# Kernel optimization log

Hardware: AMD Instinct MI355X
Metric: run time of the kernel (lower is better)

## Reference

```python
import jax, jax.numpy as jnp
import numpy as np

N = 8          # num merged RadialMLPs (experts)
D_IN = 64      # in_features
H = 128        # hidden_features
D_OUT = 64     # out_features
E = 100000     # num edges
LN_EPS = 1e-5


def setup_inputs() -> dict:
    key = jax.random.key(0)
    ks = jax.random.split(key, 12)
    s = lambda *shape: 0.05
    return {
        "x": jax.random.normal(ks[0], (E, D_IN), dtype=jnp.float32),
        # first layer concatenated across experts: [N*H, D_IN]
        "W1_cat": jax.random.normal(ks[1], (N * H, D_IN), dtype=jnp.float32) * 0.05,
        "b1_cat": jax.random.normal(ks[2], (N * H,), dtype=jnp.float32) * 0.05,
        "gamma1": jnp.ones((N, H), dtype=jnp.float32),
        "beta1": jnp.zeros((N, H), dtype=jnp.float32),
        "W2": jax.random.normal(ks[3], (N, H, H), dtype=jnp.float32) * 0.05,
        "b2": jax.random.normal(ks[4], (N, H), dtype=jnp.float32) * 0.05,
        "gamma2": jnp.ones((N, H), dtype=jnp.float32),
        "beta2": jnp.zeros((N, H), dtype=jnp.float32),
        "W3": jax.random.normal(ks[5], (N, D_OUT, H), dtype=jnp.float32) * 0.05,
        "b3": jax.random.normal(ks[6], (N, D_OUT), dtype=jnp.float32) * 0.05,
    }


def _layer_norm(h, gamma, beta):
    # h: [E, N, H]; gamma/beta: [N, H]; normalize over last dim (biased var)
    mu = jnp.mean(h, axis=-1, keepdims=True)
    var = jnp.mean(jnp.square(h - mu), axis=-1, keepdims=True)
    hn = (h - mu) * jax.lax.rsqrt(var + LN_EPS)
    return hn * gamma[None, :, :] + beta[None, :, :]


def reference(x, W1_cat, b1_cat, gamma1, beta1, W2, b2, gamma2, beta2, W3, b3):
    # Shared first GEMM: [E, D_IN] x [D_IN, N*H] -> [E, N, H]
    h = (x @ W1_cat.T + b1_cat).reshape(x.shape[0], N, H)
    h = jax.nn.silu(_layer_norm(h, gamma1, beta1))
    # Per-expert Linear 2, batched: W2 is [N, H_out, H_in]
    h = jnp.einsum("enh,nkh->enk", h, W2) + b2[None, :, :]
    h = jax.nn.silu(_layer_norm(h, gamma2, beta2))
    # Per-expert Linear 3: W3 is [N, D_OUT, H]
    out = jnp.einsum("enh,noh->eno", h, W3) + b3[None, :, :]
    # [N, E, D_OUT]: stack of the N per-expert outputs (original returns a list)
    return jnp.transpose(out, (1, 0, 2))
```

## Files before the change

kernel.cpp:

```cpp
#include <hip/hip_runtime.h>

#define NEXP 8
#define E_TOT 100000
#define EPB 64
#define NTILE 1563

typedef __bf16 bf16x8 __attribute__((ext_vector_type(8)));
typedef float f32x4 __attribute__((ext_vector_type(4)));
typedef unsigned short u16x8 __attribute__((ext_vector_type(8)));

union BF8 { u16x8 u; bf16x8 b; };
union BW  { __bf16 h; unsigned short u; };

__device__ __forceinline__ unsigned short f2bf(float f) {
  unsigned int u = __float_as_uint(f);
  u += 0x7fffu + ((u >> 16) & 1u);
  return (unsigned short)(u >> 16);
}

__device__ __forceinline__ int sidx(int r, int c, int stride) {
  return r * stride + (c ^ ((r & 7) << 3));
}

__device__ __forceinline__ bf16x8 fragld(const unsigned short* a, int off) {
  BF8 t;
  t.u = *(const u16x8*)(a + off);
  return t.b;
}

__device__ __forceinline__ bf16x8 frag_f32(const float* s) {
  float4 u0 = *(const float4*)s;
  float4 u1 = *(const float4*)(s + 4);
  BF8 t;
  t.u[0]=f2bf(u0.x); t.u[1]=f2bf(u0.y); t.u[2]=f2bf(u0.z); t.u[3]=f2bf(u0.w);
  t.u[4]=f2bf(u1.x); t.u[5]=f2bf(u1.y); t.u[6]=f2bf(u1.z); t.u[7]=f2bf(u1.w);
  return t.b;
}

__global__ void k_conv_w(const float* __restrict__ W1c, const float* __restrict__ W2p,
                         const float* __restrict__ W3p, unsigned short* __restrict__ wsW) {
  int gid = blockIdx.x * 256 + threadIdx.x;
  int n = gid >> 15, p = gid & 32767;
  int idx, frag, t, s;
  const float* base;
  int K;
  if (p < 8192)       { idx = p;         frag = idx >> 9; t = frag >> 1; s = frag & 1;
                        base = W1c + (size_t)n * 8192;  K = 64; }
  else if (p < 24576) { idx = p - 8192;  frag = idx >> 9; t = frag >> 2; s = frag & 3;
                        base = W2p + (size_t)n * 16384; K = 128; }
  else                { idx = p - 24576; frag = idx >> 9; t = frag >> 2; s = frag & 3;
                        base = W3p + (size_t)n * 8192;  K = 128; }
  int r = idx & 511, lane = r >> 3, j = r & 7;
  int l15 = lane & 15, gq = lane >> 4;
  wsW[gid] = f2bf(base[(16 * t + l15) * K + 32 * s + 8 * gq + j]);
}

__global__ void k_conv_x(const float* __restrict__ xg, unsigned short* __restrict__ xb) {
  int gid = blockIdx.x * 256 + threadIdx.x;
  const float* s = xg + (size_t)gid * 8;
  BF8 t;
  float4 a = *(const float4*)s, b = *(const float4*)(s + 4);
  t.u[0]=f2bf(a.x); t.u[1]=f2bf(a.y); t.u[2]=f2bf(a.z); t.u[3]=f2bf(a.w);
  t.u[4]=f2bf(b.x); t.u[5]=f2bf(b.y); t.u[6]=f2bf(b.z); t.u[7]=f2bf(b.w);
  *(u16x8*)(xb + (size_t)gid * 8) = t.u;
}

template <bool USEWS>
__global__ __launch_bounds__(256, 3) void k_main(
    const unsigned short* __restrict__ wsW, const unsigned short* __restrict__ xb,
    const float* __restrict__ xg,
    const float* __restrict__ W1c, const float* __restrict__ b1c,
    const float* __restrict__ g1p, const float* __restrict__ bt1p,
    const float* __restrict__ W2p, const float* __restrict__ b2p,
    const float* __restrict__ g2p, const float* __restrict__ bt2p,
    const float* __restrict__ W3p, const float* __restrict__ b3p,
    float* __restrict__ outp)
{
  __shared__ __attribute__((aligned(16))) unsigned short hs[EPB * 128];
  __shared__ __attribute__((aligned(16))) float prm[832];

  const int bid = blockIdx.x;
  const int g_  = (bid & 7) * NTILE + (bid >> 3);
  const int tile = g_ >> 3;
  const int n    = g_ & 7;
  const int e0   = tile * EPB;

  const int tid  = threadIdx.x;
  const int lane = tid & 63;
  const int wv   = tid >> 6;
  const int l15  = lane & 15;
  const int gq   = lane >> 4;
  const int wrow = wv * 16;

  for (int i = tid; i < 832; i += 256) {
    int grp = i >> 7, f = i & 127;
    float v;
    switch (grp) {
      case 0: v = b1c [n * 128 + f]; break;
      case 1: v = g1p [n * 128 + f]; break;
      case 2: v = bt1p[n * 128 + f]; break;
      case 3: v = b2p [n * 128 + f]; break;
      case 4: v = g2p [n * 128 + f]; break;
      case 5: v = bt2p[n * 128 + f]; break;
      default: v = b3p[n * 64 + f]; break;
    }
    prm[i] = v;
  }

  bf16x8 ax[2];
  {
    int e = e0 + wrow + l15;
    if (e >= E_TOT) e = E_TOT - 1;
    if (USEWS) {
#pragma unroll
      for (int s = 0; s < 2; ++s)
        ax[s] = fragld(xb, e * 64 + s * 32 + 8 * gq);
    } else {
#pragma unroll
      for (int s = 0; s < 2; ++s)
        ax[s] = frag_f32(xg + (size_t)e * 64 + s * 32 + 8 * gq);
    }
  }

  const unsigned short* wf1 = wsW + (size_t)n * 32768;
  const unsigned short* wf2 = wf1 + 8192;
  const unsigned short* wf3 = wf1 + 24576;
  const float* W1n = W1c + (size_t)n * 8192;
  const float* W2n = W2p + (size_t)n * 16384;
  const float* W3n = W3p + (size_t)n * 8192;

  auto wfragA = [&](const unsigned short* wf, const float* Wn, int nfs, int t, int s, int K) {
    if (USEWS) return fragld(wf, ((t * nfs + s) << 9) + (lane << 3));
    return frag_f32(Wn + (16 * t + l15) * K + 32 * s + 8 * gq);
  };

  __syncthreads();

  f32x4 acc[8];

  auto ln_silu_store = [&](int pb) {
    f32x4 sm4 = acc[0];
    f32x4 sq4 = acc[0] * acc[0];
#pragma unroll
    for (int ct = 1; ct < 8; ++ct) {
      f32x4 v = acc[ct];
      sm4 += v;
      sq4 += v * v;
    }
#pragma unroll
    for (int m = 1; m <= 8; m <<= 1) {
      f32x4 so, qo;
#pragma unroll
      for (int j = 0; j < 4; ++j) {
        so[j] = __shfl_xor(sm4[j], m);
        qo[j] = __shfl_xor(sq4[j], m);
      }
      sm4 += so;
      sq4 += qo;
    }
    f32x4 mu  = sm4 * (1.f / 128.f);
    f32x4 var = sq4 * (1.f / 128.f) - mu * mu;
    f32x4 rs;
#pragma unroll
    for (int j = 0; j < 4; ++j) rs[j] = __builtin_amdgcn_rsqf(var[j] + 1e-5f);
    int r0 = wrow + 4 * gq;
#pragma unroll
    for (int ct = 0; ct < 8; ++ct) {
      float gv  = prm[pb + 128 + 16 * ct + l15];
      float btv = prm[pb + 256 + 16 * ct + l15];
      f32x4 t = (acc[ct] - mu) * rs;
#pragma unroll
      for (int j = 0; j < 4; ++j) {
        float v = t[j] * gv + btv;
        v = v * __builtin_amdgcn_rcpf(1.f + __expf(-v));
        BW bw; bw.h = (__bf16)v;
        hs[sidx(r0 + j, ct * 16 + l15, 128)] = bw.u;
      }
    }
  };

#pragma unroll
  for (int ct = 0; ct < 8; ++ct) {
    float bv = prm[16 * ct + l15];
    f32x4 b4 = {bv, bv, bv, bv};
    acc[ct] = b4;
  }
#pragma unroll
  for (int s = 0; s < 2; ++s) {
#pragma unroll
    for (int ct = 0; ct < 8; ++ct) {
      bf16x8 b = wfragA(wf1, W1n, 2, ct, s, 64);
      acc[ct] = __builtin_amdgcn_mfma_f32_16x16x32_bf16(ax[s], b, acc[ct], 0, 0, 0);
    }
  }
  ln_silu_store(0);

  f32x4 acc2[8];
#pragma unroll
  for (int ct = 0; ct < 8; ++ct) {
    float bv = prm[384 + 16 * ct + l15];
    f32x4 b4 = {bv, bv, bv, bv};
    acc2[ct] = b4;
  }
#pragma unroll
  for (int ks = 0; ks < 4; ++ks) {
    bf16x8 a0 = fragld(hs, sidx(wrow + l15, ks * 32 + 8 * gq, 128));
#pragma unroll
    for (int ct = 0; ct < 8; ++ct) {
      bf16x8 b = wfragA(wf2, W2n, 4, ct, ks, 128);
      acc2[ct] = __builtin_amdgcn_mfma_f32_16x16x32_bf16(a0, b, acc2[ct], 0, 0, 0);
    }
  }
#pragma unroll
  for (int ct = 0; ct < 8; ++ct) acc[ct] = acc2[ct];
  ln_silu_store(384);

  f32x4 a3[4];
#pragma unroll
  for (int ct = 0; ct < 4; ++ct) {
    float bv = prm[768 + 16 * ct + l15];
    f32x4 b4 = {bv, bv, bv, bv};
    a3[ct] = b4;
  }
#pragma unroll
  for (int ks = 0; ks < 4; ++ks) {
    bf16x8 a0 = fragld(hs, sidx(wrow + l15, ks * 32 + 8 * gq, 128));
#pragma unroll
    for (int ct = 0; ct < 4; ++ct) {
      bf16x8 b = wfragA(wf3, W3n, 4, ct, ks, 128);
      a3[ct] = __builtin_amdgcn_mfma_f32_16x16x32_bf16(a0, b, a3[ct], 0, 0, 0);
    }
  }

#pragma unroll
  for (int j = 0; j < 4; ++j) {
    int e = e0 + wrow + 4 * gq + j;
    if (e < E_TOT) {
      float* po = outp + ((size_t)n * E_TOT + e) * 64 + l15;
#pragma unroll
      for (int ct = 0; ct < 4; ++ct)
        po[ct * 16] = a3[ct][j];
    }
  }
}

extern "C" void kernel_launch(void* const* d_in, const int* in_sizes, int n_in,
                              void* d_out, int out_size, void* d_ws, size_t ws_size,
                              hipStream_t stream) {
  (void)in_sizes; (void)n_in; (void)out_size;
  const float* xg   = (const float*)d_in[0];
  const float* W1c  = (const float*)d_in[1];
  const float* b1c  = (const float*)d_in[2];
  const float* g1p  = (const float*)d_in[3];
  const float* bt1p = (const float*)d_in[4];
  const float* W2p  = (const float*)d_in[5];
  const float* b2p  = (const float*)d_in[6];
  const float* g2p  = (const float*)d_in[7];
  const float* bt2p = (const float*)d_in[8];
  const float* W3p  = (const float*)d_in[9];
  const float* b3p  = (const float*)d_in[10];
  float* outp = (float*)d_out;

  const size_t WS_W = (size_t)NEXP * 32768 * sizeof(unsigned short);
  const size_t WS_X = (size_t)E_TOT * 64 * sizeof(unsigned short);
  const bool usews = ws_size >= WS_W + WS_X;

  dim3 grid(NEXP * NTILE, 1, 1);
  dim3 block(256, 1, 1);

  if (usews) {
    unsigned short* wsW = (unsigned short*)d_ws;
    unsigned short* xb  = wsW + (size_t)NEXP * 32768;
    k_conv_w<<<1024, 256, 0, stream>>>(W1c, W2p, W3p, wsW);
    k_conv_x<<<3125, 256, 0, stream>>>(xg, xb);
    k_main<true><<<grid, block, 0, stream>>>(wsW, xb, xg, W1c, b1c, g1p, bt1p,
                                             W2p, b2p, g2p, bt2p, W3p, b3p, outp);
  } else {
    k_main<false><<<grid, block, 0, stream>>>(nullptr, nullptr, xg, W1c, b1c, g1p, bt1p,
                                              W2p, b2p, g2p, bt2p, W3p, b3p, outp);
  }
}
```

Baseline: 173.6 us.

## Permute W3 output columns for float4 stores and keep LN params in registers

```diff
diff --git a/kernel.cpp b/kernel.cpp
--- a/kernel.cpp
+++ b/kernel.cpp
@@ -41,7 +41,7 @@
                          const float* __restrict__ W3p, unsigned short* __restrict__ wsW) {
   int gid = blockIdx.x * 256 + threadIdx.x;
   int n = gid >> 15, p = gid & 32767;
-  int idx, frag, t, s;
+  int idx, frag, t, s, row;
   const float* base;
   int K;
   if (p < 8192)       { idx = p;         frag = idx >> 9; t = frag >> 1; s = frag & 1;
@@ -52,7 +52,8 @@
                         base = W3p + (size_t)n * 8192;  K = 128; }
   int r = idx & 511, lane = r >> 3, j = r & 7;
   int l15 = lane & 15, gq = lane >> 4;
-  wsW[gid] = f2bf(base[(16 * t + l15) * K + 32 * s + 8 * gq + j]);
+  row = (p < 24576) ? (16 * t + l15) : (4 * l15 + t);
+  wsW[gid] = f2bf(base[row * K + 32 * s + 8 * gq + j]);
 }
 
 __global__ void k_conv_x(const float* __restrict__ xg, unsigned short* __restrict__ xb) {
@@ -77,7 +78,6 @@
     float* __restrict__ outp)
 {
   __shared__ __attribute__((aligned(16))) unsigned short hs[EPB * 128];
-  __shared__ __attribute__((aligned(16))) float prm[832];
 
   const int bid = blockIdx.x;
   const int g_  = (bid & 7) * NTILE + (bid >> 3);
@@ -92,20 +92,14 @@
   const int gq   = lane >> 4;
   const int wrow = wv * 16;
 
-  for (int i = tid; i < 832; i += 256) {
-    int grp = i >> 7, f = i & 127;
-    float v;
-    switch (grp) {
-      case 0: v = b1c [n * 128 + f]; break;
-      case 1: v = g1p [n * 128 + f]; break;
-      case 2: v = bt1p[n * 128 + f]; break;
-      case 3: v = b2p [n * 128 + f]; break;
-      case 4: v = g2p [n * 128 + f]; break;
-      case 5: v = bt2p[n * 128 + f]; break;
-      default: v = b3p[n * 64 + f]; break;
-    }
-    prm[i] = v;
-  }
+  float b1v[8], g1v[8], bt1v[8], b2v[8], g2v[8], bt2v[8];
+#pragma unroll
+  for (int ct = 0; ct < 8; ++ct) {
+    int col = n * 128 + ct * 16 + l15;
+    b1v[ct] = b1c[col];  g1v[ct] = g1p[col];  bt1v[ct] = bt1p[col];
+    b2v[ct] = b2p[col];  g2v[ct] = g2p[col];  bt2v[ct] = bt2p[col];
+  }
+  float4 b34 = *(const float4*)(b3p + n * 64 + 4 * l15);
 
   bf16x8 ax[2];
   {
@@ -129,16 +123,14 @@
   const float* W2n = W2p + (size_t)n * 16384;
   const float* W3n = W3p + (size_t)n * 8192;
 
-  auto wfragA = [&](const unsigned short* wf, const float* Wn, int nfs, int t, int s, int K) {
-    if (USEWS) return fragld(wf, ((t * nfs + s) << 9) + (lane << 3));
-    return frag_f32(Wn + (16 * t + l15) * K + 32 * s + 8 * gq);
+  auto wfrag = [&](const unsigned short* wf, const float* Wn, int fidx, int row, int s, int K) {
+    if (USEWS) return fragld(wf, (fidx << 9) + (lane << 3));
+    return frag_f32(Wn + row * K + 32 * s + 8 * gq);
   };
 
-  __syncthreads();
-
   f32x4 acc[8];
 
-  auto ln_silu_store = [&](int pb) {
+  auto ln_silu_store = [&](const float (&gv)[8], const float (&btv)[8]) {
     f32x4 sm4 = acc[0];
     f32x4 sq4 = acc[0] * acc[0];
 #pragma unroll
@@ -166,12 +158,10 @@
     int r0 = wrow + 4 * gq;
 #pragma unroll
     for (int ct = 0; ct < 8; ++ct) {
-      float gv  = prm[pb + 128 + 16 * ct + l15];
-      float btv = prm[pb + 256 + 16 * ct + l15];
       f32x4 t = (acc[ct] - mu) * rs;
 #pragma unroll
       for (int j = 0; j < 4; ++j) {
-        float v = t[j] * gv + btv;
+        float v = t[j] * gv[ct] + btv[ct];
         v = v * __builtin_amdgcn_rcpf(1.f + __expf(-v));
         BW bw; bw.h = (__bf16)v;
         hs[sidx(r0 + j, ct * 16 + l15, 128)] = bw.u;
@@ -181,7 +171,7 @@
 
 #pragma unroll
   for (int ct = 0; ct < 8; ++ct) {
-    float bv = prm[16 * ct + l15];
+    float bv = b1v[ct];
     f32x4 b4 = {bv, bv, bv, bv};
     acc[ct] = b4;
   }
@@ -189,16 +179,16 @@
   for (int s = 0; s < 2; ++s) {
 #pragma unroll
     for (int ct = 0; ct < 8; ++ct) {
-      bf16x8 b = wfragA(wf1, W1n, 2, ct, s, 64);
+      bf16x8 b = wfrag(wf1, W1n, ct * 2 + s, 16 * ct + l15, s, 64);
       acc[ct] = __builtin_amdgcn_mfma_f32_16x16x32_bf16(ax[s], b, acc[ct], 0, 0, 0);
     }
   }
-  ln_silu_store(0);
+  ln_silu_store(g1v, bt1v);
 
   f32x4 acc2[8];
 #pragma unroll
   for (int ct = 0; ct < 8; ++ct) {
-    float bv = prm[384 + 16 * ct + l15];
+    float bv = b2v[ct];
     f32x4 b4 = {bv, bv, bv, bv};
     acc2[ct] = b4;
   }
@@ -207,28 +197,28 @@
     bf16x8 a0 = fragld(hs, sidx(wrow + l15, ks * 32 + 8 * gq, 128));
 #pragma unroll
     for (int ct = 0; ct < 8; ++ct) {
-      bf16x8 b = wfragA(wf2, W2n, 4, ct, ks, 128);
+      bf16x8 b = wfrag(wf2, W2n, ct * 4 + ks, 16 * ct + l15, ks, 128);
       acc2[ct] = __builtin_amdgcn_mfma_f32_16x16x32_bf16(a0, b, acc2[ct], 0, 0, 0);
     }
   }
 #pragma unroll
   for (int ct = 0; ct < 8; ++ct) acc[ct] = acc2[ct];
-  ln_silu_store(384);
+  ln_silu_store(g2v, bt2v);
 
   f32x4 a3[4];
 #pragma unroll
-  for (int ct = 0; ct < 4; ++ct) {
-    float bv = prm[768 + 16 * ct + l15];
+  for (int t = 0; t < 4; ++t) {
+    float bv = ((const float*)&b34)[t];
     f32x4 b4 = {bv, bv, bv, bv};
-    a3[ct] = b4;
+    a3[t] = b4;
   }
 #pragma unroll
   for (int ks = 0; ks < 4; ++ks) {
     bf16x8 a0 = fragld(hs, sidx(wrow + l15, ks * 32 + 8 * gq, 128));
 #pragma unroll
-    for (int ct = 0; ct < 4; ++ct) {
-      bf16x8 b = wfragA(wf3, W3n, 4, ct, ks, 128);
-      a3[ct] = __builtin_amdgcn_mfma_f32_16x16x32_bf16(a0, b, a3[ct], 0, 0, 0);
+    for (int t = 0; t < 4; ++t) {
+      bf16x8 b = wfrag(wf3, W3n, t * 4 + ks, 4 * l15 + t, ks, 128);
+      a3[t] = __builtin_amdgcn_mfma_f32_16x16x32_bf16(a0, b, a3[t], 0, 0, 0);
     }
   }
 
@@ -236,10 +226,9 @@
   for (int j = 0; j < 4; ++j) {
     int e = e0 + wrow + 4 * gq + j;
     if (e < E_TOT) {
-      float* po = outp + ((size_t)n * E_TOT + e) * 64 + l15;
-#pragma unroll
-      for (int ct = 0; ct < 4; ++ct)
-        po[ct * 16] = a3[ct][j];
+      float4 o4;
+      o4.x = a3[0][j]; o4.y = a3[1][j]; o4.z = a3[2][j]; o4.w = a3[3][j];
+      *(float4*)(outp + ((size_t)n * E_TOT + e) * 64 + 4 * l15) = o4;
     }
   }
 }
```

Measured after the change: 167.8 us. -3.3%, faster.
